# Kernel optimization log

Hardware: AMD Instinct MI355X
Metric: run time of the kernel (lower is better)

The kernel has to match this reference:

```python
import jax, jax.numpy as jnp
import numpy as np

N_NODES = 100000
N_EDGES = 1600000
D_IN = 128
D_HID = 128
LATENT = 64
N_GRAPHS = 512


def setup_inputs() -> dict:
    key = jax.random.key(0)
    ks = jax.random.split(key, 10)
    x = jax.random.normal(ks[0], (N_NODES, D_IN), dtype=jnp.float32)
    edge_index = jax.random.randint(ks[1], (2, N_EDGES), 0, N_NODES, dtype=jnp.int64)
    batch = jnp.sort(jax.random.randint(ks[2], (N_NODES,), 0, N_GRAPHS, dtype=jnp.int64))
    def lin(k, fan_in, fan_out):
        return jax.random.normal(k, (fan_in, fan_out), dtype=jnp.float32) / np.sqrt(fan_in)
    W1 = lin(ks[3], D_IN, D_HID); b1 = jnp.zeros((D_HID,), jnp.float32)
    W2 = lin(ks[4], D_HID, D_HID); b2 = jnp.zeros((D_HID,), jnp.float32)
    W3 = lin(ks[5], D_HID, 2 * LATENT); b3 = jnp.zeros((2 * LATENT,), jnp.float32)
    return {"x": x, "edge_index": edge_index, "batch": batch,
            "W1": W1, "b1": b1, "W2": W2, "b2": b2, "W3": W3, "b3": b3}


def _gcn_norm(edge_index, n_nodes):
    # PyG GCNConv default: add self-loops, symmetric normalization
    loop = jnp.arange(n_nodes, dtype=edge_index.dtype)
    src = jnp.concatenate([edge_index[0], loop])
    dst = jnp.concatenate([edge_index[1], loop])
    deg = jax.ops.segment_sum(jnp.ones_like(dst, dtype=jnp.float32), dst,
                              num_segments=n_nodes)
    dinv = jnp.where(deg > 0, jax.lax.rsqrt(deg), 0.0)
    norm = dinv[src] * dinv[dst]  # [E + N]
    return src, dst, norm


def _gcn_conv(x, W, b, src, dst, norm, n_nodes):
    h = x @ W                               # [N, d_out]
    msg = h[src] * norm[:, None]            # gather + scale, [E+N, d_out]
    agg = jax.ops.segment_sum(msg, dst, num_segments=n_nodes)
    return agg + b


def reference(x, edge_index, batch, W1, b1, W2, b2, W3, b3):
    n = x.shape[0]
    src, dst, norm = _gcn_norm(edge_index, n)
    h = jax.nn.relu(_gcn_conv(x, W1, b1, src, dst, norm, n))
    h = jax.nn.relu(_gcn_conv(h, W2, b2, src, dst, norm, n))
    h = _gcn_conv(h, W3, b3, src, dst, norm, n)
    # scatter_mean over batch ids -> [num_graphs, 2*latent]
    cnt = jax.ops.segment_sum(jnp.ones((n,), jnp.float32), batch,
                              num_segments=N_GRAPHS)
    summed = jax.ops.segment_sum(h, batch, num_segments=N_GRAPHS)
    return summed / jnp.maximum(cnt, 1.0)[:, None]
```

## Files before the change

### kernel.cpp

```cpp
#include <hip/hip_runtime.h>
#include <stdint.h>

typedef unsigned short u16;
typedef unsigned int   u32;

#define N_NODES  100000
#define N_EDGES  1600000
#define DFEAT    128
#define N_GRAPHS 512

#define NBKT   391
#define NBLK_E 782
#define LBUF   8192

typedef float f32x4 __attribute__((ext_vector_type(4)));
typedef short s16x8 __attribute__((ext_vector_type(8)));

__device__ __forceinline__ float bflo(u32 u) { return __uint_as_float(u << 16); }
__device__ __forceinline__ float bfhi(u32 u) { return __uint_as_float(u & 0xffff0000u); }
__device__ __forceinline__ u16 f2bf(float f) {
  u32 u = __float_as_uint(f);
  return (u16)((u + 0x7fffu + ((u >> 16) & 1u)) >> 16);
}
__device__ __forceinline__ u32 pack2(float f0, float f1) {
  return (u32)f2bf(f0) | ((u32)f2bf(f1) << 16);
}

__device__ __forceinline__ int ld_src(const int* ei, int m, int e) {
  return m ? ei[2 * e] : ei[e];
}
__device__ __forceinline__ int ld_dst(const int* ei, int m, int e) {
  return m ? ei[2 * (N_EDGES + e)] : ei[N_EDGES + e];
}

__global__ __launch_bounds__(256) void prep_k(const int* __restrict__ ei, int* __restrict__ flag,
                                              const float* __restrict__ W1, const float* __restrict__ W2,
                                              const float* __restrict__ W3, u16* __restrict__ T1,
                                              u16* __restrict__ T2, u16* __restrict__ T3) {
  int t = threadIdx.x;
  if (blockIdx.x == 0) {
    if (t < 64) {
      int v = ei[2 * t + 1];
      unsigned long long m = __ballot(v != 0);
      if (t == 0) *flag = (m == 0ull) ? 1 : 0;
    }
    return;
  }
  const float* W = (blockIdx.x == 1) ? W1 : (blockIdx.x == 2) ? W2 : W3;
  u16* T         = (blockIdx.x == 1) ? T1 : (blockIdx.x == 2) ? T2 : T3;
  for (int i = t; i < DFEAT * DFEAT; i += 256) {
    int n = i >> 7, k = i & 127;
    T[i] = f2bf(W[k * DFEAT + n]);
  }
}


__global__ __launch_bounds__(256) void histA_k(const int* __restrict__ ei,
                                               const int* __restrict__ flag,
                                               int* __restrict__ ghist) {
  __shared__ int hist[NBKT];
  int t = threadIdx.x, b = blockIdx.x;
  for (int i = t; i < NBKT; i += 256) hist[i] = 0;
  __syncthreads();
  int m = *flag;
  int e0 = b * 2048;
#pragma unroll
  for (int p = 0; p < 8; p++) {
    int e = e0 + p * 256 + t;
    if (e < N_EDGES) atomicAdd(&hist[ld_dst(ei, m, e) >> 8], 1);
  }
  __syncthreads();
  for (int i = t; i < NBKT; i += 256) ghist[b * NBKT + i] = hist[i];
}

__global__ __launch_bounds__(256) void scanB1_k(int* __restrict__ ghist,
                                                int* __restrict__ gtot) {
  __shared__ int a[1024];
  __shared__ int ts[256];
  int t = threadIdx.x, k = blockIdx.x;
  for (int i = t; i < 1024; i += 256) a[i] = (i < NBLK_E) ? ghist[i * NBKT + k] : 0;
  __syncthreads();
  int b4 = t * 4;
  int x0 = a[b4], x1 = a[b4 + 1], x2 = a[b4 + 2], x3 = a[b4 + 3];
  int tot = x0 + x1 + x2 + x3;
  ts[t] = tot;
  for (int off = 1; off < 256; off <<= 1) {
    __syncthreads(); int add = (t >= off) ? ts[t - off] : 0;
    __syncthreads(); ts[t] += add;
  }
  __syncthreads();
  int excl = ts[t] - tot;
  a[b4] = excl; a[b4 + 1] = excl + x0; a[b4 + 2] = excl + x0 + x1; a[b4 + 3] = excl + x0 + x1 + x2;
  __syncthreads();
  for (int i = t; i < NBLK_E; i += 256) ghist[i * NBKT + k] = a[i];
  if (t == 255) gtot[k] = ts[255];
}

__global__ __launch_bounds__(512) void scanB2_k(const int* __restrict__ gtot,
                                                int* __restrict__ bbase) {
  __shared__ int tmp[512];
  int t = threadIdx.x;
  int v = (t < NBKT) ? gtot[t] : 0;
  tmp[t] = v;
  for (int off = 1; off < 512; off <<= 1) {
    __syncthreads(); int add = (t >= off) ? tmp[t - off] : 0;
    __syncthreads(); tmp[t] += add;
  }
  __syncthreads();
  if (t < NBKT) bbase[t] = tmp[t] - v;
  if (t == 0) bbase[NBKT] = N_EDGES;
}

__global__ __launch_bounds__(256) void scatterC_k(const int* __restrict__ ei,
                                                  const int* __restrict__ flag,
                                                  const int* __restrict__ obase,
                                                  const int* __restrict__ bbase,
                                                  u32* __restrict__ colpk) {
  __shared__ int cur[NBKT];
  int t = threadIdx.x, b = blockIdx.x;
  for (int i = t; i < NBKT; i += 256) cur[i] = bbase[i] + obase[b * NBKT + i];
  __syncthreads();
  int m = *flag;
  int e0 = b * 2048;
#pragma unroll
  for (int p = 0; p < 8; p++) {
    int e = e0 + p * 256 + t;
    if (e < N_EDGES) {
      int d = ld_dst(ei, m, e);
      int s = ld_src(ei, m, e);
      int pos = atomicAdd(&cur[d >> 8], 1);
      colpk[pos] = (u32)s | ((u32)(d & 255) << 24);
    }
  }
}

__global__ __launch_bounds__(256) void fillD_k(const int* __restrict__ bbase,
                                               const u32* __restrict__ colpk,
                                               int* __restrict__ colarr,
                                               int* __restrict__ rowptr,
                                               float* __restrict__ dinv) {
  __shared__ int hist[256];
  __shared__ int cur[256];
  __shared__ int lbuf[LBUF];
  int t = threadIdx.x, b = blockIdx.x;
  int base = bbase[b], end = bbase[b + 1], cnt = end - base;
  hist[t] = 0;
  __syncthreads();
  for (int i = t; i < cnt; i += 256) atomicAdd(&hist[colpk[base + i] >> 24], 1);
  __syncthreads();
  int c = hist[t];
  cur[t] = c;
  for (int off = 1; off < 256; off <<= 1) {
    __syncthreads(); int add = (t >= off) ? cur[t - off] : 0;
    __syncthreads(); cur[t] += add;
  }
  __syncthreads();
  int excl = cur[t] - c;
  int node = b * 256 + t;
  if (node < N_NODES) {
    rowptr[node] = base + excl;
    dinv[node] = rsqrtf((float)(c + 1));
  }
  if (b == NBKT - 1 && t == 0) rowptr[N_NODES] = N_EDGES;
  __syncthreads();
  cur[t] = excl;
  __syncthreads();
  for (int i = t; i < cnt; i += 256) {
    u32 v = colpk[base + i];
    int slot = atomicAdd(&cur[v >> 24], 1);
    if (slot < LBUF) lbuf[slot] = (int)(v & 0x00FFFFFFu);
  }
  __syncthreads();
  for (int i = t; i < cnt; i += 256) colarr[base + i] = lbuf[i];
}

#define LP 136

__global__ __launch_bounds__(256, 1) void gemm_scale_k(const void* __restrict__ Xv,
                                                       int x_is_f32,
                                                       const u16* __restrict__ Wt,
                                                       const float* __restrict__ dinv,
                                                       u16* __restrict__ Y, int nrows) {
  __shared__ u16 sX[128 * LP];
  __shared__ u16 sW[128 * LP];
  int tid = threadIdx.x;
  int r0 = blockIdx.x * 128;

  for (int c = tid; c < 2048; c += 256) {
    int row = c >> 4, off = (c & 15) * 8;
    *(uint4*)(&sW[row * LP + off]) = *(const uint4*)(Wt + row * DFEAT + off);
  }
  if (x_is_f32) {
    const float* Xf = (const float*)Xv;
    for (int c = tid; c < 2048; c += 256) {
      int row = c >> 4, off = (c & 15) * 8;
      int grow = r0 + row;
      uint4 o = make_uint4(0, 0, 0, 0);
      if (grow < nrows) {
        const float* px = Xf + (size_t)grow * DFEAT + off;
        float4 v0 = *(const float4*)px;
        float4 v1 = *(const float4*)(px + 4);
        o.x = pack2(v0.x, v0.y); o.y = pack2(v0.z, v0.w);
        o.z = pack2(v1.x, v1.y); o.w = pack2(v1.z, v1.w);
      }
      *(uint4*)(&sX[row * LP + off]) = o;
    }
  } else {
    const u16* Xb = (const u16*)Xv;
    for (int c = tid; c < 2048; c += 256) {
      int row = c >> 4, off = (c & 15) * 8;
      int grow = r0 + row;
      uint4 v = make_uint4(0, 0, 0, 0);
      if (grow < nrows) v = *(const uint4*)(Xb + (size_t)grow * DFEAT + off);
      *(uint4*)(&sX[row * LP + off]) = v;
    }
  }
  __syncthreads();

  int wave = tid >> 6, lane = tid & 63;
  int q = lane >> 4, r = lane & 15;
  int wr0 = wave * 32;

  f32x4 acc[2][8];
#pragma unroll
  for (int m = 0; m < 2; m++)
#pragma unroll
    for (int i = 0; i < 8; i++) acc[m][i] = (f32x4){0.f, 0.f, 0.f, 0.f};

#pragma unroll
  for (int kk = 0; kk < 4; kk++) {
    int k0 = kk * 32;
    s16x8 a0 = *(const s16x8*)(&sX[(wr0 + r) * LP + k0 + q * 8]);
    s16x8 a1 = *(const s16x8*)(&sX[(wr0 + 16 + r) * LP + k0 + q * 8]);
#pragma unroll
    for (int nt = 0; nt < 8; nt++) {
      s16x8 b = *(const s16x8*)(&sW[(nt * 16 + r) * LP + k0 + q * 8]);
      acc[0][nt] = __builtin_amdgcn_mfma_f32_16x16x32_bf16(a0, b, acc[0][nt], 0, 0, 0);
      acc[1][nt] = __builtin_amdgcn_mfma_f32_16x16x32_bf16(a1, b, acc[1][nt], 0, 0, 0);
    }
  }

#pragma unroll
  for (int m = 0; m < 2; m++) {
#pragma unroll
    for (int i = 0; i < 4; i++) {
      int grow = r0 + wr0 + m * 16 + q * 4 + i;
      if (grow < nrows) {
        float dv = dinv[grow];
#pragma unroll
        for (int nt = 0; nt < 8; nt++) {
          Y[(size_t)grow * DFEAT + nt * 16 + r] = f2bf(acc[m][nt][i] * dv);
        }
      }
    }
  }
}

struct Acc8 {
  float a0, a1, a2, a3, a4, a5, a6, a7;
  __device__ __forceinline__ void add(uint4 v) {
    a0 += bflo(v.x); a1 += bfhi(v.x); a2 += bflo(v.y); a3 += bfhi(v.y);
    a4 += bflo(v.z); a5 += bfhi(v.z); a6 += bflo(v.w); a7 += bfhi(v.w);
  }
};

__global__ __launch_bounds__(256) void agg_k(const u32* __restrict__ HS,
                                             const float* __restrict__ dinv,
                                             const int* __restrict__ rowptr,
                                             const int* __restrict__ colidx,
                                             const float* __restrict__ bias,
                                             u32* __restrict__ OUT, int do_relu) {
  int t = threadIdx.x;
  int node = blockIdx.x * 16 + (t >> 4);
  int fp = t & 15;

  int s = rowptr[node], e = rowptr[node + 1];

  Acc8 A;
  uint4 v = *(const uint4*)(HS + (size_t)node * 64 + fp * 4);
  A.a0 = bflo(v.x); A.a1 = bfhi(v.x); A.a2 = bflo(v.y); A.a3 = bfhi(v.y);
  A.a4 = bflo(v.z); A.a5 = bfhi(v.z); A.a6 = bflo(v.w); A.a7 = bfhi(v.w);

  for (int w = s; w < e; w += 16) {
    int c = (w + fp < e) ? colidx[w + fp] : 0;
    int n = min(16, e - w);
    int j = 0;
    for (; j + 8 <= n; j += 8) {
      int i0 = __shfl(c, j, 16),     i1 = __shfl(c, j + 1, 16);
      int i2 = __shfl(c, j + 2, 16), i3 = __shfl(c, j + 3, 16);
      int i4 = __shfl(c, j + 4, 16), i5 = __shfl(c, j + 5, 16);
      int i6 = __shfl(c, j + 6, 16), i7 = __shfl(c, j + 7, 16);
      uint4 w0 = *(const uint4*)(HS + (size_t)i0 * 64 + fp * 4);
      uint4 w1 = *(const uint4*)(HS + (size_t)i1 * 64 + fp * 4);
      uint4 w2 = *(const uint4*)(HS + (size_t)i2 * 64 + fp * 4);
      uint4 w3 = *(const uint4*)(HS + (size_t)i3 * 64 + fp * 4);
      uint4 w4 = *(const uint4*)(HS + (size_t)i4 * 64 + fp * 4);
      uint4 w5 = *(const uint4*)(HS + (size_t)i5 * 64 + fp * 4);
      uint4 w6 = *(const uint4*)(HS + (size_t)i6 * 64 + fp * 4);
      uint4 w7 = *(const uint4*)(HS + (size_t)i7 * 64 + fp * 4);
      A.add(w0); A.add(w1); A.add(w2); A.add(w3);
      A.add(w4); A.add(w5); A.add(w6); A.add(w7);
    }
    for (; j + 4 <= n; j += 4) {
      int i0 = __shfl(c, j, 16),     i1 = __shfl(c, j + 1, 16);
      int i2 = __shfl(c, j + 2, 16), i3 = __shfl(c, j + 3, 16);
      uint4 w0 = *(const uint4*)(HS + (size_t)i0 * 64 + fp * 4);
      uint4 w1 = *(const uint4*)(HS + (size_t)i1 * 64 + fp * 4);
      uint4 w2 = *(const uint4*)(HS + (size_t)i2 * 64 + fp * 4);
      uint4 w3 = *(const uint4*)(HS + (size_t)i3 * 64 + fp * 4);
      A.add(w0); A.add(w1); A.add(w2); A.add(w3);
    }
    for (; j < n; j++) {
      int i0 = __shfl(c, j, 16);
      uint4 w0 = *(const uint4*)(HS + (size_t)i0 * 64 + fp * 4);
      A.add(w0);
    }
  }

  float dv = dinv[node];
  float4 b0 = *(const float4*)(bias + fp * 8);
  float4 b1 = *(const float4*)(bias + fp * 8 + 4);
  float r0 = A.a0 * dv + b0.x, r1 = A.a1 * dv + b0.y;
  float r2 = A.a2 * dv + b0.z, r3 = A.a3 * dv + b0.w;
  float r4 = A.a4 * dv + b1.x, r5 = A.a5 * dv + b1.y;
  float r6 = A.a6 * dv + b1.z, r7 = A.a7 * dv + b1.w;
  if (do_relu) {
    r0 = fmaxf(r0, 0.f); r1 = fmaxf(r1, 0.f); r2 = fmaxf(r2, 0.f); r3 = fmaxf(r3, 0.f);
    r4 = fmaxf(r4, 0.f); r5 = fmaxf(r5, 0.f); r6 = fmaxf(r6, 0.f); r7 = fmaxf(r7, 0.f);
  }
  uint4 o;
  o.x = pack2(r0, r1); o.y = pack2(r2, r3); o.z = pack2(r4, r5); o.w = pack2(r6, r7);
  *(uint4*)(OUT + (size_t)node * 64 + fp * 4) = o;
}

__device__ __forceinline__ int lower_bound_i(const int* a, int n, int key, int shift) {
  int lo = 0, hi = n;
  while (lo < hi) {
    int mid = (lo + hi) >> 1;
    if (a[mid << shift] < key) lo = mid + 1; else hi = mid;
  }
  return lo;
}

__global__ __launch_bounds__(256) void pool_k(const u32* __restrict__ H,
                                              const int* __restrict__ batch,
                                              const int* __restrict__ flag,
                                              float* __restrict__ OUT) {
  int g = blockIdx.x;
  int m = *flag;
  int lo = lower_bound_i(batch, N_NODES, g, m);
  int hi = lower_bound_i(batch, N_NODES, g + 1, m);
  int cnt = hi - lo;
  int d2 = threadIdx.x & 63;
  int half = threadIdx.x >> 6;
  float a0 = 0.f, a1 = 0.f;
  for (int row = lo + half; row < hi; row += 4) {
    u32 v = H[(size_t)row * 64 + d2];
    a0 += bflo(v); a1 += bfhi(v);
  }
  __shared__ float red0[256], red1[256];
  red0[threadIdx.x] = a0; red1[threadIdx.x] = a1;
  __syncthreads();
  if (threadIdx.x < 64) {
    float s0 = red0[d2] + red0[d2 + 64] + red0[d2 + 128] + red0[d2 + 192];
    float s1 = red1[d2] + red1[d2 + 64] + red1[d2 + 128] + red1[d2 + 192];
    float inv = 1.0f / fmaxf((float)cnt, 1.0f);
    OUT[g * DFEAT + 2 * d2]     = s0 * inv;
    OUT[g * DFEAT + 2 * d2 + 1] = s1 * inv;
  }
}


extern "C" void kernel_launch(void* const* d_in, const int* in_sizes, int n_in,
                              void* d_out, int out_size, void* d_ws, size_t ws_size,
                              hipStream_t stream) {
  const float* x   = (const float*)d_in[0];
  const int* ei    = (const int*)d_in[1];
  const int* batch = (const int*)d_in[2];
  const float* W1  = (const float*)d_in[3];
  const float* b1  = (const float*)d_in[4];
  const float* W2  = (const float*)d_in[5];
  const float* b2  = (const float*)d_in[6];
  const float* W3  = (const float*)d_in[7];
  const float* b3  = (const float*)d_in[8];
  float* out = (float*)d_out;

  char* p = (char*)d_ws;
  size_t off = 0;
  auto carve = [&](size_t bytes) -> void* {
    void* q = p + off;
    off = (off + bytes + 255) & ~(size_t)255;
    return q;
  };
  int*   flag   = (int*)carve(256);
  int*   ghist  = (int*)carve((size_t)NBLK_E * NBKT * 4);
  int*   gtot   = (int*)carve(NBKT * 4);
  int*   bbase  = (int*)carve((NBKT + 1) * 4);
  int*   rowptr = (int*)carve((N_NODES + 1) * 4);
  float* dinv   = (float*)carve(N_NODES * 4);
  u32*   colpk  = (u32*)carve((size_t)N_EDGES * 4);
  int*   colarr = (int*)carve((size_t)N_EDGES * 4);
  u16*   Wt1    = (u16*)carve(DFEAT * DFEAT * 2);
  u16*   Wt2    = (u16*)carve(DFEAT * DFEAT * 2);
  u16*   Wt3    = (u16*)carve(DFEAT * DFEAT * 2);
  u32*   bufA   = (u32*)carve((size_t)N_NODES * 64 * 4);
  u32*   bufB   = (u32*)carve((size_t)N_NODES * 64 * 4);
  (void)ws_size;

  prep_k<<<4, 256, 0, stream>>>(ei, flag, W1, W2, W3, Wt1, Wt2, Wt3);
  histA_k<<<NBLK_E, 256, 0, stream>>>(ei, flag, ghist);
  scanB1_k<<<NBKT, 256, 0, stream>>>(ghist, gtot);
  scanB2_k<<<1, 512, 0, stream>>>(gtot, bbase);
  scatterC_k<<<NBLK_E, 256, 0, stream>>>(ei, flag, ghist, bbase, colpk);
  fillD_k<<<NBKT, 256, 0, stream>>>(bbase, colpk, colarr, rowptr, dinv);

  const int GB = (N_NODES + 127) / 128;
  const int AB = N_NODES / 16;

  gemm_scale_k<<<GB, 256, 0, stream>>>((const void*)x, 1, Wt1, dinv, (u16*)bufA, N_NODES);
  agg_k<<<AB, 256, 0, stream>>>(bufA, dinv, rowptr, colarr, b1, bufB, 1);
  gemm_scale_k<<<GB, 256, 0, stream>>>((const void*)bufB, 0, Wt2, dinv, (u16*)bufA, N_NODES);
  agg_k<<<AB, 256, 0, stream>>>(bufA, dinv, rowptr, colarr, b2, bufB, 1);
  gemm_scale_k<<<GB, 256, 0, stream>>>((const void*)bufB, 0, Wt3, dinv, (u16*)bufA, N_NODES);
  agg_k<<<AB, 256, 0, stream>>>(bufA, dinv, rowptr, colarr, b3, bufB, 0);
  pool_k<<<N_GRAPHS, 256, 0, stream>>>(bufB, batch, flag, out);
}
```

Measured before the change: 412.9 us.

## Fuse aggregation with next-layer GEMM and fold bucket scan into consumers

Layers one and two now run a single kernel that gathers neighbour rows, applies bias and ReLU into shared memory, then multiplies by the next weight matrix with MFMA and scales by dinv. This avoids writing the intermediate activations to global memory and reading them back, and removes one launch per layer. The single-block bucket-total scan kernel is also removed, and every scatter and fill block recomputes that scan itself to save a launch. The cost is redundant scan work in each of those blocks and a larger-LDS, 512-thread fused kernel that may run at lower occupancy during the latency-bound gather.

```diff
diff --git a/kernel.cpp b/kernel.cpp
--- a/kernel.cpp
+++ b/kernel.cpp
@@ -96,29 +96,42 @@
   if (t == 255) gtot[k] = ts[255];
 }
 
-__global__ __launch_bounds__(512) void scanB2_k(const int* __restrict__ gtot,
-                                                int* __restrict__ bbase) {
-  __shared__ int tmp[512];
+__device__ __forceinline__ void scan_gtot_block(const int* __restrict__ gtot,
+                                                int* bb, int* sc) {
   int t = threadIdx.x;
-  int v = (t < NBKT) ? gtot[t] : 0;
-  tmp[t] = v;
-  for (int off = 1; off < 512; off <<= 1) {
-    __syncthreads(); int add = (t >= off) ? tmp[t - off] : 0;
-    __syncthreads(); tmp[t] += add;
-  }
-  __syncthreads();
-  if (t < NBKT) bbase[t] = tmp[t] - v;
-  if (t == 0) bbase[NBKT] = N_EDGES;
+  int v0 = gtot[t];
+  sc[t] = v0;
+  for (int off = 1; off < 256; off <<= 1) {
+    __syncthreads(); int add = (t >= off) ? sc[t - off] : 0;
+    __syncthreads(); sc[t] += add;
+  }
+  __syncthreads();
+  bb[t] = sc[t] - v0;
+  int base256 = sc[255];
+  __syncthreads();
+  int v1 = (t < NBKT - 256) ? gtot[256 + t] : 0;
+  sc[t] = v1;
+  for (int off = 1; off < 256; off <<= 1) {
+    __syncthreads(); int add = (t >= off) ? sc[t - off] : 0;
+    __syncthreads(); sc[t] += add;
+  }
+  __syncthreads();
+  if (t < NBKT - 256) bb[256 + t] = base256 + sc[t] - v1;
+  if (t == 0) bb[NBKT] = N_EDGES;
+  __syncthreads();
 }
 
 __global__ __launch_bounds__(256) void scatterC_k(const int* __restrict__ ei,
                                                   const int* __restrict__ flag,
                                                   const int* __restrict__ obase,
-                                                  const int* __restrict__ bbase,
+                                                  const int* __restrict__ gtot,
                                                   u32* __restrict__ colpk) {
   __shared__ int cur[NBKT];
+  __shared__ int bb[NBKT + 1];
+  __shared__ int sc[256];
   int t = threadIdx.x, b = blockIdx.x;
-  for (int i = t; i < NBKT; i += 256) cur[i] = bbase[i] + obase[b * NBKT + i];
+  scan_gtot_block(gtot, bb, sc);
+  for (int i = t; i < NBKT; i += 256) cur[i] = bb[i] + obase[b * NBKT + i];
   __syncthreads();
   int m = *flag;
   int e0 = b * 2048;
@@ -134,7 +147,7 @@
   }
 }
 
-__global__ __launch_bounds__(256) void fillD_k(const int* __restrict__ bbase,
+__global__ __launch_bounds__(256) void fillD_k(const int* __restrict__ gtot,
                                                const u32* __restrict__ colpk,
                                                int* __restrict__ colarr,
                                                int* __restrict__ rowptr,
@@ -142,8 +155,11 @@
   __shared__ int hist[256];
   __shared__ int cur[256];
   __shared__ int lbuf[LBUF];
+  __shared__ int bb[NBKT + 1];
+  __shared__ int sc[256];
   int t = threadIdx.x, b = blockIdx.x;
-  int base = bbase[b], end = bbase[b + 1], cnt = end - base;
+  scan_gtot_block(gtot, bb, sc);
+  int base = bb[b], end = bb[b + 1], cnt = end - base;
   hist[t] = 0;
   __syncthreads();
   for (int i = t; i < cnt; i += 256) atomicAdd(&hist[colpk[base + i] >> 24], 1);
@@ -176,8 +192,7 @@
 
 #define LP 136
 
-__global__ __launch_bounds__(256, 1) void gemm_scale_k(const void* __restrict__ Xv,
-                                                       int x_is_f32,
+__global__ __launch_bounds__(256, 1) void gemm_scale_k(const float* __restrict__ Xf,
                                                        const u16* __restrict__ Wt,
                                                        const float* __restrict__ dinv,
                                                        u16* __restrict__ Y, int nrows) {
@@ -190,30 +205,18 @@
     int row = c >> 4, off = (c & 15) * 8;
     *(uint4*)(&sW[row * LP + off]) = *(const uint4*)(Wt + row * DFEAT + off);
   }
-  if (x_is_f32) {
-    const float* Xf = (const float*)Xv;
-    for (int c = tid; c < 2048; c += 256) {
-      int row = c >> 4, off = (c & 15) * 8;
-      int grow = r0 + row;
-      uint4 o = make_uint4(0, 0, 0, 0);
-      if (grow < nrows) {
-        const float* px = Xf + (size_t)grow * DFEAT + off;
-        float4 v0 = *(const float4*)px;
-        float4 v1 = *(const float4*)(px + 4);
-        o.x = pack2(v0.x, v0.y); o.y = pack2(v0.z, v0.w);
-        o.z = pack2(v1.x, v1.y); o.w = pack2(v1.z, v1.w);
-      }
-      *(uint4*)(&sX[row * LP + off]) = o;
-    }
-  } else {
-    const u16* Xb = (const u16*)Xv;
-    for (int c = tid; c < 2048; c += 256) {
-      int row = c >> 4, off = (c & 15) * 8;
-      int grow = r0 + row;
-      uint4 v = make_uint4(0, 0, 0, 0);
-      if (grow < nrows) v = *(const uint4*)(Xb + (size_t)grow * DFEAT + off);
-      *(uint4*)(&sX[row * LP + off]) = v;
-    }
+  for (int c = tid; c < 2048; c += 256) {
+    int row = c >> 4, off = (c & 15) * 8;
+    int grow = r0 + row;
+    uint4 o = make_uint4(0, 0, 0, 0);
+    if (grow < nrows) {
+      const float* px = Xf + (size_t)grow * DFEAT + off;
+      float4 v0 = *(const float4*)px;
+      float4 v1 = *(const float4*)(px + 4);
+      o.x = pack2(v0.x, v0.y); o.y = pack2(v0.z, v0.w);
+      o.z = pack2(v1.x, v1.y); o.w = pack2(v1.z, v1.w);
+    }
+    *(uint4*)(&sX[row * LP + off]) = o;
   }
   __syncthreads();
 
@@ -264,23 +267,15 @@
   }
 };
 
-__global__ __launch_bounds__(256) void agg_k(const u32* __restrict__ HS,
-                                             const float* __restrict__ dinv,
-                                             const int* __restrict__ rowptr,
-                                             const int* __restrict__ colidx,
-                                             const float* __restrict__ bias,
-                                             u32* __restrict__ OUT, int do_relu) {
-  int t = threadIdx.x;
-  int node = blockIdx.x * 16 + (t >> 4);
-  int fp = t & 15;
-
+__device__ __forceinline__ Acc8 gather_row(const u32* __restrict__ HS,
+                                           const int* __restrict__ rowptr,
+                                           const int* __restrict__ colidx,
+                                           int node, int fp) {
   int s = rowptr[node], e = rowptr[node + 1];
-
   Acc8 A;
   uint4 v = *(const uint4*)(HS + (size_t)node * 64 + fp * 4);
   A.a0 = bflo(v.x); A.a1 = bfhi(v.x); A.a2 = bflo(v.y); A.a3 = bfhi(v.y);
   A.a4 = bflo(v.z); A.a5 = bfhi(v.z); A.a6 = bflo(v.w); A.a7 = bfhi(v.w);
-
   for (int w = s; w < e; w += 16) {
     int c = (w + fp < e) ? colidx[w + fp] : 0;
     int n = min(16, e - w);
@@ -316,6 +311,92 @@
       A.add(w0);
     }
   }
+  return A;
+}
+
+__global__ __launch_bounds__(512) void agg_gemm_k(const u32* __restrict__ HS,
+                                                  const float* __restrict__ dinv,
+                                                  const int* __restrict__ rowptr,
+                                                  const int* __restrict__ colidx,
+                                                  const float* __restrict__ bias,
+                                                  const u16* __restrict__ Wt,
+                                                  u16* __restrict__ Y) {
+  __shared__ u16 sX[64 * LP];
+  __shared__ u16 sW[128 * LP];
+  int tid = threadIdx.x;
+  int r0 = blockIdx.x * 64;
+
+  for (int c = tid; c < 2048; c += 512) {
+    int row = c >> 4, off = (c & 15) * 8;
+    *(uint4*)(&sW[row * LP + off]) = *(const uint4*)(Wt + row * DFEAT + off);
+  }
+
+  int g = tid >> 4, fp = tid & 15;
+  float4 b0 = *(const float4*)(bias + fp * 8);
+  float4 b1 = *(const float4*)(bias + fp * 8 + 4);
+#pragma unroll
+  for (int j = 0; j < 2; j++) {
+    int lrow = g * 2 + j;
+    int node = r0 + lrow;
+    uint4 o = make_uint4(0, 0, 0, 0);
+    if (node < N_NODES) {
+      Acc8 A = gather_row(HS, rowptr, colidx, node, fp);
+      float dv = dinv[node];
+      float r0f = fmaxf(A.a0 * dv + b0.x, 0.f), r1f = fmaxf(A.a1 * dv + b0.y, 0.f);
+      float r2f = fmaxf(A.a2 * dv + b0.z, 0.f), r3f = fmaxf(A.a3 * dv + b0.w, 0.f);
+      float r4f = fmaxf(A.a4 * dv + b1.x, 0.f), r5f = fmaxf(A.a5 * dv + b1.y, 0.f);
+      float r6f = fmaxf(A.a6 * dv + b1.z, 0.f), r7f = fmaxf(A.a7 * dv + b1.w, 0.f);
+      o.x = pack2(r0f, r1f); o.y = pack2(r2f, r3f);
+      o.z = pack2(r4f, r5f); o.w = pack2(r6f, r7f);
+    }
+    *(uint4*)(&sX[lrow * LP + fp * 8]) = o;
+  }
+  __syncthreads();
+
+  int wave = tid >> 6, lane = tid & 63;
+  int q = lane >> 4, r = lane & 15;
+  int mt = wave >> 1;
+  int nt0 = (wave & 1) * 4;
+
+  f32x4 acc[4];
+#pragma unroll
+  for (int i = 0; i < 4; i++) acc[i] = (f32x4){0.f, 0.f, 0.f, 0.f};
+
+#pragma unroll
+  for (int kk = 0; kk < 4; kk++) {
+    int k0 = kk * 32;
+    s16x8 a = *(const s16x8*)(&sX[(mt * 16 + r) * LP + k0 + q * 8]);
+#pragma unroll
+    for (int nt = 0; nt < 4; nt++) {
+      s16x8 b = *(const s16x8*)(&sW[((nt0 + nt) * 16 + r) * LP + k0 + q * 8]);
+      acc[nt] = __builtin_amdgcn_mfma_f32_16x16x32_bf16(a, b, acc[nt], 0, 0, 0);
+    }
+  }
+
+#pragma unroll
+  for (int i = 0; i < 4; i++) {
+    int grow = r0 + mt * 16 + q * 4 + i;
+    if (grow < N_NODES) {
+      float dv = dinv[grow];
+#pragma unroll
+      for (int nt = 0; nt < 4; nt++) {
+        Y[(size_t)grow * DFEAT + (nt0 + nt) * 16 + r] = f2bf(acc[nt][i] * dv);
+      }
+    }
+  }
+}
+
+__global__ __launch_bounds__(256) void agg_k(const u32* __restrict__ HS,
+                                             const float* __restrict__ dinv,
+                                             const int* __restrict__ rowptr,
+                                             const int* __restrict__ colidx,
+                                             const float* __restrict__ bias,
+                                             u32* __restrict__ OUT, int do_relu) {
+  int t = threadIdx.x;
+  int node = blockIdx.x * 16 + (t >> 4);
+  int fp = t & 15;
+
+  Acc8 A = gather_row(HS, rowptr, colidx, node, fp);
 
   float dv = dinv[node];
   float4 b0 = *(const float4*)(bias + fp * 8);
@@ -395,7 +476,6 @@
   int*   flag   = (int*)carve(256);
   int*   ghist  = (int*)carve((size_t)NBLK_E * NBKT * 4);
   int*   gtot   = (int*)carve(NBKT * 4);
-  int*   bbase  = (int*)carve((NBKT + 1) * 4);
   int*   rowptr = (int*)carve((N_NODES + 1) * 4);
   float* dinv   = (float*)carve(N_NODES * 4);
   u32*   colpk  = (u32*)carve((size_t)N_EDGES * 4);
@@ -410,18 +490,16 @@
   prep_k<<<4, 256, 0, stream>>>(ei, flag, W1, W2, W3, Wt1, Wt2, Wt3);
   histA_k<<<NBLK_E, 256, 0, stream>>>(ei, flag, ghist);
   scanB1_k<<<NBKT, 256, 0, stream>>>(ghist, gtot);
-  scanB2_k<<<1, 512, 0, stream>>>(gtot, bbase);
-  scatterC_k<<<NBLK_E, 256, 0, stream>>>(ei, flag, ghist, bbase, colpk);
-  fillD_k<<<NBKT, 256, 0, stream>>>(bbase, colpk, colarr, rowptr, dinv);
+  scatterC_k<<<NBLK_E, 256, 0, stream>>>(ei, flag, ghist, gtot, colpk);
+  fillD_k<<<NBKT, 256, 0, stream>>>(gtot, colpk, colarr, rowptr, dinv);
 
   const int GB = (N_NODES + 127) / 128;
+  const int FB = (N_NODES + 63) / 64;
   const int AB = N_NODES / 16;
 
-  gemm_scale_k<<<GB, 256, 0, stream>>>((const void*)x, 1, Wt1, dinv, (u16*)bufA, N_NODES);
-  agg_k<<<AB, 256, 0, stream>>>(bufA, dinv, rowptr, colarr, b1, bufB, 1);
-  gemm_scale_k<<<GB, 256, 0, stream>>>((const void*)bufB, 0, Wt2, dinv, (u16*)bufA, N_NODES);
-  agg_k<<<AB, 256, 0, stream>>>(bufA, dinv, rowptr, colarr, b2, bufB, 1);
-  gemm_scale_k<<<GB, 256, 0, stream>>>((const void*)bufB, 0, Wt3, dinv, (u16*)bufA, N_NODES);
+  gemm_scale_k<<<GB, 256, 0, stream>>>(x, Wt1, dinv, (u16*)bufA, N_NODES);
+  agg_gemm_k<<<FB, 512, 0, stream>>>(bufA, dinv, rowptr, colarr, b1, Wt2, (u16*)bufB);
+  agg_gemm_k<<<FB, 512, 0, stream>>>(bufB, dinv, rowptr, colarr, b2, Wt3, (u16*)bufA);
   agg_k<<<AB, 256, 0, stream>>>(bufA, dinv, rowptr, colarr, b3, bufB, 0);
   pool_k<<<N_GRAPHS, 256, 0, stream>>>(bufB, batch, flag, out);
 }
```

New measurement: 411.2 us. About the same (-0.4%).
